# Performance work log

Measured on AMD Instinct MI355X. Metric: run time of the kernel, lower is better.

The kernel has to match this reference:

```python
import jax, jax.numpy as jnp
import numpy as np

N = 50000      # nodes
E = 1600000    # edges
IN = 128       # in_channels
H = 64         # hidden_channels
P = 200000     # edge pairs to score
BN_EPS = 1e-5


def setup_inputs() -> dict:
    key = jax.random.key(0)
    ks = jax.random.split(key, 24)
    lin = lambda k, i, o: jax.random.normal(k, (i, o), jnp.float32) / np.sqrt(i).astype(np.float32)
    return {
        "x": jax.random.normal(ks[0], (N, IN), jnp.float32),
        "edge_index": jax.random.randint(ks[1], (2, E), 0, N, jnp.int32),
        "src": jax.random.randint(ks[2], (P,), 0, N, jnp.int32),
        "dst": jax.random.randint(ks[3], (P,), 0, N, jnp.int32),
        # GCNConv weights/biases
        "W1": lin(ks[4], IN, H),        "b1": jnp.zeros((H,), jnp.float32),
        "W2": lin(ks[5], H, 2 * H),     "b2": jnp.zeros((2 * H,), jnp.float32),
        "W3": lin(ks[6], 2 * H, 2 * H), "b3": jnp.zeros((2 * H,), jnp.float32),
        # BatchNorm affine params
        "g1": jnp.ones((H,), jnp.float32),     "bt1": jnp.zeros((H,), jnp.float32),
        "g2": jnp.ones((2 * H,), jnp.float32), "bt2": jnp.zeros((2 * H,), jnp.float32),
        "g3": jnp.ones((2 * H,), jnp.float32), "bt3": jnp.zeros((2 * H,), jnp.float32),
        # edge-scoring MLP: Linear(4H -> 2H), ReLU, Linear(2H -> 1)
        "fcW1": lin(ks[7], 4 * H, 2 * H), "fcb1": jnp.zeros((2 * H,), jnp.float32),
        "fcW2": lin(ks[8], 2 * H, 1),     "fcb2": jnp.zeros((1,), jnp.float32),
    }


def _gcn_norm(edge_index):
    # add self-loops, symmetric normalization D^-1/2 (A+I) D^-1/2
    loop = jnp.arange(N, dtype=edge_index.dtype)
    row = jnp.concatenate([edge_index[0], loop])
    col = jnp.concatenate([edge_index[1], loop])
    deg = jax.ops.segment_sum(jnp.ones(row.shape, jnp.float32), col, num_segments=N)
    dis = jnp.where(deg > 0, jax.lax.rsqrt(deg), 0.0)
    norm = dis[row] * dis[col]
    return row, col, norm


def _conv(x, W, b, row, col, norm):
    h = x @ W                                  # [N, C]
    msg = h[row] * norm[:, None]               # [E+N, C] gather + scale
    agg = jax.ops.segment_sum(msg, col, num_segments=N)
    return agg + b


def _bn(x, g, bt):
    mu = x.mean(0)
    var = x.var(0)
    return g * (x - mu) * jax.lax.rsqrt(var + BN_EPS) + bt


def reference(x, edge_index, src, dst,
              W1, b1, W2, b2, W3, b3,
              g1, bt1, g2, bt2, g3, bt3,
              fcW1, fcb1, fcW2, fcb2):
    row, col, norm = _gcn_norm(edge_index)
    # inference path: dropout is identity; BN uses batch statistics
    z = _bn(jax.nn.relu(_conv(x, W1, b1, row, col, norm)), g1, bt1)
    z = _bn(jax.nn.relu(_conv(z, W2, b2, row, col, norm)), g2, bt2)
    z = _bn(jax.nn.relu(_conv(z, W3, b3, row, col, norm)), g3, bt3)
    # score(): gather-concat-MLP over edge pairs
    emb = jnp.concatenate([z[src], z[dst]], axis=1)   # [P, 4H]
    hidden = jax.nn.relu(emb @ fcW1 + fcb1)
    scores = (hidden @ fcW2 + fcb2).squeeze(-1)       # [P]
    return scores
```

## Files before the change

kernel.cpp:

```cpp
#include <hip/hip_runtime.h>
#include <math.h>

typedef short bf16x8 __attribute__((ext_vector_type(8)));
typedef float f32x4 __attribute__((ext_vector_type(4)));

__device__ inline unsigned int f2bf_pack(float lo, float hi) {
    unsigned int ul = __builtin_bit_cast(unsigned int, lo);
    unsigned int uh = __builtin_bit_cast(unsigned int, hi);
    ul = ul + 0x7fffu + ((ul >> 16) & 1u);
    uh = uh + 0x7fffu + ((uh >> 16) & 1u);
    return (ul >> 16) | (uh & 0xffff0000u);
}
__device__ inline unsigned short f2bf(float f) {
    unsigned int u = __builtin_bit_cast(unsigned int, f);
    u = u + 0x7fffu + ((u >> 16) & 1u);
    return (unsigned short)(u >> 16);
}
__device__ inline float bf2f(unsigned short u) {
    return __builtin_bit_cast(float, (unsigned int)u << 16);
}
__device__ inline float bflo(unsigned int w) { return __builtin_bit_cast(float, w << 16); }
__device__ inline float bfhi(unsigned int w) { return __builtin_bit_cast(float, w & 0xffff0000u); }


__global__ __launch_bounds__(256) void k_count(const int* __restrict__ col, int* deg, int E) {
    int e = blockIdx.x * 256 + threadIdx.x;
    if (e < E) atomicAdd(&deg[col[e]], 1);
}

__global__ __launch_bounds__(1024) void k_scan_blk(const int* __restrict__ deg, int* __restrict__ offs,
                                                   int* __restrict__ bsum, float* __restrict__ dis, int n) {
    __shared__ int tmp[1024];
    int i = blockIdx.x * 1024 + threadIdx.x;
    int v = (i < n) ? deg[i] : 0;
    if (i < n) dis[i] = 1.0f / sqrtf((float)(v + 1));
    tmp[threadIdx.x] = v;
    __syncthreads();
    for (int off = 1; off < 1024; off <<= 1) {
        int t = (threadIdx.x >= off) ? tmp[threadIdx.x - off] : 0;
        __syncthreads();
        tmp[threadIdx.x] += t;
        __syncthreads();
    }
    if (i < n) offs[i] = tmp[threadIdx.x] - v;
    if (threadIdx.x == 1023) bsum[blockIdx.x] = tmp[1023];
}

__global__ void k_scan_top(int* bsum, int nb) {
    if (threadIdx.x == 0) {
        int acc = 0;
        for (int b = 0; b < nb; b++) { int t = bsum[b]; bsum[b] = acc; acc += t; }
        bsum[nb] = acc;
    }
}

__global__ __launch_bounds__(1024) void k_scan_add(int* __restrict__ offs, int* __restrict__ bcur,
                                                   const int* __restrict__ bsum, int n, int nb) {
    int i = blockIdx.x * 1024 + threadIdx.x;
    if (i < n) {
        int v = offs[i] + bsum[blockIdx.x];
        offs[i] = v;
        if ((i & 511) == 0) bcur[i >> 9] = v;
    }
    if (i == 0) offs[n] = bsum[nb];
}


__global__ __launch_bounds__(256) void k_binA(const int* __restrict__ row, const int* __restrict__ col,
                                              int* __restrict__ bcur, int2* __restrict__ binned,
                                              int E, int NB) {
    constexpr int SLOTS = 32;
    constexpr int CHUNK = 2048;
    __shared__ int2 stage[128][SLOTS];
    __shared__ int lcount[128];
    for (int b = threadIdx.x; b < 128; b += 256) lcount[b] = 0;
    __syncthreads();
    for (int cs = blockIdx.x * CHUNK; cs < E; cs += gridDim.x * CHUNK) {
#pragma unroll
        for (int j = 0; j < CHUNK / 256; ++j) {
            int e = cs + j * 256 + threadIdx.x;
            if (e < E) {
                int r = row[e], c = col[e];
                int b = c >> 9;
                int pos = atomicAdd(&lcount[b], 1);
                if (pos < SLOTS) stage[b][pos] = make_int2(r, c);
                else {
                    int gp = atomicAdd(&bcur[b], 1);
                    binned[gp] = make_int2(r, c);
                }
            }
        }
        __syncthreads();
        for (int b = threadIdx.x; b < NB; b += 256) {
            int c = lcount[b];
            if (c > SLOTS) c = SLOTS;
            if (c > 0) {
                int gp = atomicAdd(&bcur[b], c);
                for (int j = 0; j < c; ++j) binned[gp + j] = stage[b][j];
            }
            lcount[b] = 0;
        }
        __syncthreads();
    }
}

__global__ __launch_bounds__(1024) void k_binB(const int2* __restrict__ binned, const int* __restrict__ offs,
                                               const float* __restrict__ dis, int2* __restrict__ csr, int N) {
    constexpr int CAP = 17408;
    __shared__ int2 stage[CAP];
    __shared__ int cnt[512];
    __shared__ int cur[512];
    const int b = blockIdx.x;
    const int lo = b << 9;
    int hi = lo + 512; if (hi > N) hi = N;
    const int base = offs[lo];
    const int total = offs[hi] - base;

    if (threadIdx.x < 512) cnt[threadIdx.x] = 0;
    __syncthreads();
    for (int i = threadIdx.x; i < total; i += 1024)
        atomicAdd(&cnt[binned[base + i].y - lo], 1);
    __syncthreads();
    int own = 0;
    if (threadIdx.x < 512) own = cnt[threadIdx.x];
    for (int off = 1; off < 512; off <<= 1) {
        int t = 0;
        if (threadIdx.x < 512 && threadIdx.x >= off) t = cnt[threadIdx.x - off];
        __syncthreads();
        if (threadIdx.x < 512) cnt[threadIdx.x] += t;
        __syncthreads();
    }
    if (threadIdx.x < 512) cur[threadIdx.x] = cnt[threadIdx.x] - own;
    __syncthreads();
    for (int i = threadIdx.x; i < total; i += 1024) {
        int2 e = binned[base + i];
        int slot = atomicAdd(&cur[e.y - lo], 1);
        int2 o = make_int2(e.x, __builtin_bit_cast(int, dis[e.x]));
        if (slot < CAP) stage[slot] = o;
        else csr[base + slot] = o;
    }
    __syncthreads();
    int lim = total < CAP ? total : CAP;
    for (int i = threadIdx.x; i < lim; i += 1024) csr[base + i] = stage[i];
}


__global__ __launch_bounds__(256) void k_cast(const float* __restrict__ X, unsigned short* __restrict__ Y, int n8) {
    int i = blockIdx.x * 256 + threadIdx.x;
    if (i >= n8) return;
    const float4* x4 = (const float4*)X;
    float4 a = x4[2 * i], b = x4[2 * i + 1];
    uint4 o = make_uint4(f2bf_pack(a.x, a.y), f2bf_pack(a.z, a.w),
                         f2bf_pack(b.x, b.y), f2bf_pack(b.z, b.w));
    *(uint4*)(Y + (size_t)i * 8) = o;
}


template <int K, int COUT>
__global__ __launch_bounds__(256) void k_prep(const float* __restrict__ W, unsigned short* __restrict__ Wt) {
    constexpr int NG = (COUT / 16) * (K / 32) * 64;
    int g = blockIdx.x * 256 + threadIdx.x;
    if (g >= NG) return;
    int l = g & 63;
    int ks = (g >> 6) % (K / 32);
    int nt = g / (64 * (K / 32));
    int n = nt * 16 + (l & 15);
    int k0 = ks * 32 + (l >> 4) * 8;
    unsigned int w[4];
#pragma unroll
    for (int j = 0; j < 4; ++j) {
        float a = W[(size_t)(k0 + 2 * j) * COUT + n];
        float b = W[(size_t)(k0 + 2 * j + 1) * COUT + n];
        w[j] = f2bf_pack(a, b);
    }
    *(uint4*)(Wt + (size_t)g * 8) = make_uint4(w[0], w[1], w[2], w[3]);
}


template <int K, int COUT, bool FUSED>
__global__ __launch_bounds__(256) void k_mgemm(const unsigned short* __restrict__ Xb,
                                               const unsigned short* __restrict__ Wt,
                                               const float* __restrict__ bias,
                                               unsigned short* __restrict__ H,
                                               float* __restrict__ part, int n) {
    constexpr int NT = COUT / 16;
    constexpr int KS = K / 32;
    __shared__ float reds[FUSED ? 16 : 1][COUT];
    __shared__ float redq[FUSED ? 16 : 1][COUT];
    const int lane = threadIdx.x & 63;
    const int wave = threadIdx.x >> 6;
    const int m = lane & 15, g4 = lane >> 4;
    const int rb = blockIdx.x * 64 + wave * 16;

    bf16x8 af[KS];
    {
        int arow = rb + m;
        if (arow >= n) arow = n - 1;
        const unsigned short* xr = Xb + (size_t)arow * K + g4 * 8;
#pragma unroll
        for (int ks = 0; ks < KS; ++ks) af[ks] = *(const bf16x8*)(xr + ks * 32);
    }
    const bf16x8* Wv = (const bf16x8*)Wt;
    f32x4 acc[NT];
#pragma unroll
    for (int nt = 0; nt < NT; ++nt) {
        f32x4 a = {0.f, 0.f, 0.f, 0.f};
#pragma unroll
        for (int ks = 0; ks < KS; ++ks)
            a = __builtin_amdgcn_mfma_f32_16x16x32_bf16(af[ks], Wv[(nt * KS + ks) * 64 + lane], a, 0, 0, 0);
        acc[nt] = a;
    }

    if (!FUSED) {
#pragma unroll
        for (int nt = 0; nt < NT; ++nt)
#pragma unroll
            for (int r = 0; r < 4; ++r) {
                int gr = rb + g4 * 4 + r;
                if (gr < n) H[(size_t)gr * COUT + nt * 16 + m] = f2bf(acc[nt][r]);
            }
    } else {
        float vs[NT], vq[NT];
#pragma unroll
        for (int nt = 0; nt < NT; ++nt) {
            float b1 = bias[nt * 16 + m];
            vs[nt] = 0.f; vq[nt] = 0.f;
#pragma unroll
            for (int r = 0; r < 4; ++r) {
                int gr = rb + g4 * 4 + r;
                bool ok = gr < n;
                float val = ok ? fmaxf(acc[nt][r] + b1, 0.f) : 0.f;
                if (ok) H[(size_t)gr * COUT + nt * 16 + m] = f2bf(val);
                vs[nt] += val;
                vq[nt] += val * val;
            }
        }
#pragma unroll
        for (int nt = 0; nt < NT; ++nt) {
            reds[wave * 4 + g4][nt * 16 + m] = vs[nt];
            redq[wave * 4 + g4][nt * 16 + m] = vq[nt];
        }
        __syncthreads();
        for (int c = threadIdx.x; c < COUT; c += 256) {
            float S = 0.f, Q = 0.f;
#pragma unroll
            for (int t = 0; t < 16; ++t) { S += reds[t][c]; Q += redq[t][c]; }
            part[(size_t)blockIdx.x * 2 * COUT + c] = S;
            part[(size_t)blockIdx.x * 2 * COUT + COUT + c] = Q;
        }
    }
}


__global__ __launch_bounds__(256) void k_agg64(const unsigned short* __restrict__ H, const int* __restrict__ offs,
                                               const int2* __restrict__ csr, const float* __restrict__ dis,
                                               const float* __restrict__ bias, unsigned short* __restrict__ Y,
                                               float* __restrict__ part, int n) {
    const int lane = threadIdx.x & 63;
    const int wave = threadIdx.x >> 6;
    const int gw = blockIdx.x * 4 + wave;
    const int nw = gridDim.x * 4;
    float bsum = 0.f, bsq = 0.f;
    const float bias_r = bias[lane];

    for (int node = gw; node < n; node += nw) {
        int s0 = offs[node], s1 = offs[node + 1];
        float a = 0.f;
        int e = s0;
        for (; e + 4 <= s1; e += 4) {
            int2 e0 = csr[e], e1 = csr[e + 1], e2 = csr[e + 2], e3 = csr[e + 3];
            float h0 = bf2f(H[(size_t)e0.x * 64 + lane]);
            float h1 = bf2f(H[(size_t)e1.x * 64 + lane]);
            float h2 = bf2f(H[(size_t)e2.x * 64 + lane]);
            float h3 = bf2f(H[(size_t)e3.x * 64 + lane]);
            a += __builtin_bit_cast(float, e0.y) * h0 + __builtin_bit_cast(float, e1.y) * h1;
            a += __builtin_bit_cast(float, e2.y) * h2 + __builtin_bit_cast(float, e3.y) * h3;
        }
        for (; e < s1; ++e) {
            int2 e0 = csr[e];
            a += __builtin_bit_cast(float, e0.y) * bf2f(H[(size_t)e0.x * 64 + lane]);
        }
        float dn = dis[node];
        float val = a * dn + bf2f(H[(size_t)node * 64 + lane]) * dn * dn + bias_r;
        val = fmaxf(val, 0.f);
        Y[(size_t)node * 64 + lane] = f2bf(val);
        bsum += val;
        bsq += val * val;
    }
    __shared__ float psum[4][64], psq[4][64];
    psum[wave][lane] = bsum; psq[wave][lane] = bsq;
    __syncthreads();
    if (threadIdx.x < 64) {
        int c = threadIdx.x;
        float s = psum[0][c] + psum[1][c] + psum[2][c] + psum[3][c];
        float qq = psq[0][c] + psq[1][c] + psq[2][c] + psq[3][c];
        part[(size_t)blockIdx.x * 128 + c] = s;
        part[(size_t)blockIdx.x * 128 + 64 + c] = qq;
    }
}


template <int C>
__global__ __launch_bounds__(256) void k_aggpre(const unsigned short* __restrict__ IN, const int* __restrict__ offs,
                                                const int2* __restrict__ csr, const float* __restrict__ dis,
                                                const float* __restrict__ ss, unsigned short* __restrict__ OUT, int n) {
    constexpr int VPL = C / 64;
    const int lane = threadIdx.x & 63;
    const int wave = threadIdx.x >> 6;
    const int gw = blockIdx.x * 4 + wave;
    const int nw = gridDim.x * 4;
    float sc[VPL], sh[VPL];
#pragma unroll
    for (int q = 0; q < VPL; q++) { sc[q] = ss[lane * VPL + q]; sh[q] = ss[C + lane * VPL + q]; }

    for (int node = gw; node < n; node += nw) {
        int s0 = offs[node], s1 = offs[node + 1];
        float a[VPL];
        float S = 0.f;
#pragma unroll
        for (int q = 0; q < VPL; q++) a[q] = 0.f;
        int e = s0;
        for (; e + 4 <= s1; e += 4) {
            int2 e0 = csr[e], e1 = csr[e + 1], e2 = csr[e + 2], e3 = csr[e + 3];
            float v0 = __builtin_bit_cast(float, e0.y);
            float v1 = __builtin_bit_cast(float, e1.y);
            float v2 = __builtin_bit_cast(float, e2.y);
            float v3 = __builtin_bit_cast(float, e3.y);
            S += (v0 + v1) + (v2 + v3);
            if (VPL == 2) {
                unsigned int w0 = *(const unsigned int*)(IN + (size_t)e0.x * C + 2 * lane);
                unsigned int w1 = *(const unsigned int*)(IN + (size_t)e1.x * C + 2 * lane);
                unsigned int w2 = *(const unsigned int*)(IN + (size_t)e2.x * C + 2 * lane);
                unsigned int w3 = *(const unsigned int*)(IN + (size_t)e3.x * C + 2 * lane);
                a[0] += v0 * bflo(w0) + v1 * bflo(w1) + v2 * bflo(w2) + v3 * bflo(w3);
                a[1] += v0 * bfhi(w0) + v1 * bfhi(w1) + v2 * bfhi(w2) + v3 * bfhi(w3);
            } else {
                float h0 = bf2f(IN[(size_t)e0.x * C + lane]);
                float h1 = bf2f(IN[(size_t)e1.x * C + lane]);
                float h2 = bf2f(IN[(size_t)e2.x * C + lane]);
                float h3 = bf2f(IN[(size_t)e3.x * C + lane]);
                a[0] += v0 * h0 + v1 * h1 + v2 * h2 + v3 * h3;
            }
        }
        for (; e < s1; ++e) {
            int2 e0 = csr[e];
            float v0 = __builtin_bit_cast(float, e0.y);
            S += v0;
            if (VPL == 2) {
                unsigned int w0 = *(const unsigned int*)(IN + (size_t)e0.x * C + 2 * lane);
                a[0] += v0 * bflo(w0);
                a[1] += v0 * bfhi(w0);
            } else {
                a[0] += v0 * bf2f(IN[(size_t)e0.x * C + lane]);
            }
        }
        float dn = dis[node];
        float shf = S + dn;
        if (VPL == 2) {
            unsigned int wsf = *(const unsigned int*)(IN + (size_t)node * C + 2 * lane);
            float o0 = dn * ((a[0] + dn * bflo(wsf)) * sc[0] + shf * sh[0]);
            float o1 = dn * ((a[1] + dn * bfhi(wsf)) * sc[1] + shf * sh[1]);
            *(unsigned int*)(OUT + (size_t)node * C + 2 * lane) = f2bf_pack(o0, o1);
        } else {
            float hsf = bf2f(IN[(size_t)node * C + lane]);
            OUT[(size_t)node * C + lane] = f2bf(dn * ((a[0] + dn * hsf) * sc[0] + shf * sh[0]));
        }
    }
}


template <int C>
__global__ __launch_bounds__(1024) void k_bnfin(const float* __restrict__ part, int nblk,
                                                const float* __restrict__ g, const float* __restrict__ bt,
                                                float* __restrict__ ss, int n) {
    constexpr int ROWS = 1024 / C;
    __shared__ float ssum[1024], ssq[1024];
    const int c = threadIdx.x % C;
    const int r = threadIdx.x / C;
    float s = 0.f, q = 0.f;
    for (int b = r; b < nblk; b += ROWS) {
        s += part[(size_t)b * 2 * C + c];
        q += part[(size_t)b * 2 * C + C + c];
    }
    ssum[threadIdx.x] = s; ssq[threadIdx.x] = q;
    __syncthreads();
    if (r == 0) {
        double S = (double)s, Q = (double)q;
        for (int rr = 1; rr < ROWS; rr++) { S += (double)ssum[rr * C + c]; Q += (double)ssq[rr * C + c]; }
        double invN = 1.0 / (double)n;
        double mu = S * invN;
        double var = Q * invN - mu * mu;
        float scale = g[c] / sqrtf((float)var + 1e-5f);
        ss[c] = scale;
        ss[C + c] = bt[c] - (float)mu * scale;
    }
}


__global__ __launch_bounds__(128) void k_score(const unsigned short* __restrict__ Z, const float* __restrict__ ss,
                                               const int* __restrict__ src, const int* __restrict__ dst,
                                               const unsigned short* __restrict__ Wt,
                                               const float* __restrict__ fcb1, const float* __restrict__ fcW2,
                                               const float* __restrict__ fcb2, float* __restrict__ out, int P) {
    __shared__ unsigned int emb[2][16][128];
    const int lane = threadIdx.x & 63;
    const int wave = threadIdx.x >> 6;
    unsigned int (*Ew)[128] = emb[wave];
    const int tile = blockIdx.x * 2 + wave;
    const int pbase = tile * 16;

    const float2 sc2 = *(const float2*)&ss[2 * lane];
    const float2 sh2 = *(const float2*)&ss[128 + 2 * lane];

#pragma unroll 4
    for (int p = 0; p < 16; ++p) {
        int pi = pbase + p;
        int is = src[pi], id = dst[pi];
        unsigned int wa = *(const unsigned int*)(Z + (size_t)is * 128 + 2 * lane);
        unsigned int wb = *(const unsigned int*)(Z + (size_t)id * 128 + 2 * lane);
        unsigned int ua = f2bf_pack(bflo(wa) * sc2.x + sh2.x, bfhi(wa) * sc2.y + sh2.y);
        unsigned int ub = f2bf_pack(bflo(wb) * sc2.x + sh2.x, bfhi(wb) * sc2.y + sh2.y);
        int swz = (p & 7) << 4;
        char* rowp = (char*)&Ew[p][0];
        *(unsigned int*)(rowp + ((lane * 4) ^ swz)) = ua;
        *(unsigned int*)(rowp + (((lane + 64) * 4) ^ swz)) = ub;
    }

    const int m = lane & 15;
    const int g4 = lane >> 4;
    bf16x8 af[8];
    {
        const char* rowp = (const char*)&Ew[m][0];
        const int sw = (m & 7) << 4;
#pragma unroll
        for (int ks = 0; ks < 8; ++ks)
            af[ks] = *(const bf16x8*)(rowp + ((ks * 64 + g4 * 16) ^ sw));
    }

    float sacc[4] = {0.f, 0.f, 0.f, 0.f};
    const bf16x8* Wtv = (const bf16x8*)Wt;
#pragma unroll 2
    for (int nt = 0; nt < 8; ++nt) {
        f32x4 acc = {0.f, 0.f, 0.f, 0.f};
#pragma unroll
        for (int ks = 0; ks < 8; ++ks) {
            bf16x8 bf = Wtv[(nt * 8 + ks) * 64 + lane];
            acc = __builtin_amdgcn_mfma_f32_16x16x32_bf16(af[ks], bf, acc, 0, 0, 0);
        }
        int oc = nt * 16 + m;
        float b1 = fcb1[oc];
        float w2 = fcW2[oc];
#pragma unroll
        for (int r = 0; r < 4; ++r) {
            float h = fmaxf(acc[r] + b1, 0.f);
            sacc[r] += h * w2;
        }
    }

    const float b2v = fcb2[0];
#pragma unroll
    for (int r = 0; r < 4; ++r) {
        float s = sacc[r];
        s += __shfl_xor(s, 1);
        s += __shfl_xor(s, 2);
        s += __shfl_xor(s, 4);
        s += __shfl_xor(s, 8);
        if (m == 0) out[pbase + g4 * 4 + r] = s + b2v;
    }
}


extern "C" void kernel_launch(void* const* d_in, const int* in_sizes, int n_in,
                              void* d_out, int out_size, void* d_ws, size_t ws_size,
                              hipStream_t stream) {
    const float* x   = (const float*)d_in[0];
    const int* ei    = (const int*)d_in[1];
    const int* src   = (const int*)d_in[2];
    const int* dst   = (const int*)d_in[3];
    const float* W1  = (const float*)d_in[4];
    const float* b1  = (const float*)d_in[5];
    const float* W2  = (const float*)d_in[6];
    const float* b2  = (const float*)d_in[7];
    const float* W3  = (const float*)d_in[8];
    const float* b3  = (const float*)d_in[9];
    const float* g1  = (const float*)d_in[10];
    const float* bt1 = (const float*)d_in[11];
    const float* g2  = (const float*)d_in[12];
    const float* bt2 = (const float*)d_in[13];
    const float* g3  = (const float*)d_in[14];
    const float* bt3 = (const float*)d_in[15];
    const float* fcW1 = (const float*)d_in[16];
    const float* fcb1 = (const float*)d_in[17];
    const float* fcW2 = (const float*)d_in[18];
    const float* fcb2 = (const float*)d_in[19];
    float* out = (float*)d_out;

    const int N = in_sizes[0] / 128;
    const int E = in_sizes[1] / 2;
    const int P = in_sizes[2];
    const int* erow = ei;
    const int* ecol = ei + E;
    const int NB = (N + 511) >> 9;

    const int AGG_GRID = 2048;

    char* w = (char*)d_ws;
    auto alloc = [&](size_t bytes) { void* p = (void*)w; w += (bytes + 255) & ~(size_t)255; return p; };
    int*   deg     = (int*)alloc((size_t)N * 4);
    float* dis     = (float*)alloc((size_t)N * 4);
    int*   offs    = (int*)alloc((size_t)(N + 1) * 4);
    int*   bsum    = (int*)alloc((size_t)65 * 4);
    int*   bcur    = (int*)alloc((size_t)128 * 4);
    int2*  csr     = (int2*)alloc((size_t)E * 8);
    int2*  binned  = (int2*)alloc((size_t)E * 8);
    float* part    = (float*)alloc((size_t)AGG_GRID * 256 * 4);
    float* ss1     = (float*)alloc(2 * 64 * 4);
    float* ss2     = (float*)alloc(2 * 128 * 4);
    float* ss3     = (float*)alloc(2 * 128 * 4);
    unsigned short* Wts = (unsigned short*)alloc((size_t)4096 * 8 * 2);
    unsigned short* Wt1 = (unsigned short*)alloc((size_t)1024 * 8 * 2);
    unsigned short* Wt2 = (unsigned short*)alloc((size_t)1024 * 8 * 2);
    unsigned short* Wt3 = (unsigned short*)alloc((size_t)2048 * 8 * 2);
    unsigned short* Xb1 = (unsigned short*)alloc((size_t)N * 128 * 2);
    unsigned short* bhA = (unsigned short*)alloc((size_t)N * 128 * 2);
    unsigned short* bhB = (unsigned short*)alloc((size_t)N * 128 * 2);
    (void)ws_size; (void)n_in; (void)out_size;

    const int nb_e = (E + 255) / 256;
    const int nb_s = (N + 1023) / 1024;

    hipMemsetAsync(deg, 0, (size_t)N * 4, stream);
    k_count<<<nb_e, 256, 0, stream>>>(ecol, deg, E);
    k_scan_blk<<<nb_s, 1024, 0, stream>>>(deg, offs, bsum, dis, N);
    k_scan_top<<<1, 64, 0, stream>>>(bsum, nb_s);
    k_scan_add<<<nb_s, 1024, 0, stream>>>(offs, bcur, bsum, N, nb_s);
    k_binA<<<256, 256, 0, stream>>>(erow, ecol, bcur, binned, E, NB);
    k_binB<<<NB, 1024, 0, stream>>>(binned, offs, dis, csr, N);

    k_prep<256, 128><<<16, 256, 0, stream>>>(fcW1, Wts);
    k_prep<128, 64><<<4, 256, 0, stream>>>(W1, Wt1);
    k_prep<64, 128><<<4, 256, 0, stream>>>(W2, Wt2);
    k_prep<128, 128><<<8, 256, 0, stream>>>(W3, Wt3);
    k_cast<<<(N * 16 + 255) / 256, 256, 0, stream>>>(x, Xb1, N * 16);

    const int gemm_grid = (N + 63) / 64;

    k_mgemm<128, 64, false><<<gemm_grid, 256, 0, stream>>>(Xb1, Wt1, nullptr, bhA, nullptr, N);
    k_agg64<<<AGG_GRID, 256, 0, stream>>>(bhA, offs, csr, dis, b1, bhB, part, N);
    k_bnfin<64><<<1, 1024, 0, stream>>>(part, AGG_GRID, g1, bt1, ss1, N);

    k_aggpre<64><<<AGG_GRID, 256, 0, stream>>>(bhB, offs, csr, dis, ss1, Xb1, N);
    k_mgemm<64, 128, true><<<gemm_grid, 256, 0, stream>>>(Xb1, Wt2, b2, bhA, part, N);
    k_bnfin<128><<<1, 1024, 0, stream>>>(part, gemm_grid, g2, bt2, ss2, N);

    k_aggpre<128><<<AGG_GRID, 256, 0, stream>>>(bhA, offs, csr, dis, ss2, Xb1, N);
    k_mgemm<128, 128, true><<<gemm_grid, 256, 0, stream>>>(Xb1, Wt3, b3, bhB, part, N);
    k_bnfin<128><<<1, 1024, 0, stream>>>(part, gemm_grid, g3, bt3, ss3, N);

    const int score_grid = P / 32;
    k_score<<<score_grid, 128, 0, stream>>>(bhB, ss3, src, dst, Wts, fcb1, fcW2, fcb2, out, P);
}
```

Measured before the change: 590.3 us.

## Build CSR from fixed-capacity bucket slabs, dropping global degree count and scan

```diff
diff --git a/kernel.cpp b/kernel.cpp
--- a/kernel.cpp
+++ b/kernel.cpp
@@ -3,6 +3,8 @@
 
 typedef short bf16x8 __attribute__((ext_vector_type(8)));
 typedef float f32x4 __attribute__((ext_vector_type(4)));
+
+#define BCAP 17408
 
 __device__ inline unsigned int f2bf_pack(float lo, float hi) {
     unsigned int ul = __builtin_bit_cast(unsigned int, lo);
@@ -23,48 +25,10 @@
 __device__ inline float bfhi(unsigned int w) { return __builtin_bit_cast(float, w & 0xffff0000u); }
 
 
-__global__ __launch_bounds__(256) void k_count(const int* __restrict__ col, int* deg, int E) {
-    int e = blockIdx.x * 256 + threadIdx.x;
-    if (e < E) atomicAdd(&deg[col[e]], 1);
-}
-
-__global__ __launch_bounds__(1024) void k_scan_blk(const int* __restrict__ deg, int* __restrict__ offs,
-                                                   int* __restrict__ bsum, float* __restrict__ dis, int n) {
-    __shared__ int tmp[1024];
-    int i = blockIdx.x * 1024 + threadIdx.x;
-    int v = (i < n) ? deg[i] : 0;
-    if (i < n) dis[i] = 1.0f / sqrtf((float)(v + 1));
-    tmp[threadIdx.x] = v;
-    __syncthreads();
-    for (int off = 1; off < 1024; off <<= 1) {
-        int t = (threadIdx.x >= off) ? tmp[threadIdx.x - off] : 0;
-        __syncthreads();
-        tmp[threadIdx.x] += t;
-        __syncthreads();
-    }
-    if (i < n) offs[i] = tmp[threadIdx.x] - v;
-    if (threadIdx.x == 1023) bsum[blockIdx.x] = tmp[1023];
-}
-
-__global__ void k_scan_top(int* bsum, int nb) {
-    if (threadIdx.x == 0) {
-        int acc = 0;
-        for (int b = 0; b < nb; b++) { int t = bsum[b]; bsum[b] = acc; acc += t; }
-        bsum[nb] = acc;
-    }
-}
-
-__global__ __launch_bounds__(1024) void k_scan_add(int* __restrict__ offs, int* __restrict__ bcur,
-                                                   const int* __restrict__ bsum, int n, int nb) {
-    int i = blockIdx.x * 1024 + threadIdx.x;
-    if (i < n) {
-        int v = offs[i] + bsum[blockIdx.x];
-        offs[i] = v;
-        if ((i & 511) == 0) bcur[i >> 9] = v;
-    }
-    if (i == 0) offs[n] = bsum[nb];
-}
-
+__global__ void k_seed(int* bcur, int NB) {
+    int b = threadIdx.x;
+    if (b < NB) bcur[b] = b * BCAP;
+}
 
 __global__ __launch_bounds__(256) void k_binA(const int* __restrict__ row, const int* __restrict__ col,
                                               int* __restrict__ bcur, int2* __restrict__ binned,
@@ -104,22 +68,31 @@
     }
 }
 
-__global__ __launch_bounds__(1024) void k_binB(const int2* __restrict__ binned, const int* __restrict__ offs,
-                                               const float* __restrict__ dis, int2* __restrict__ csr, int N) {
-    constexpr int CAP = 17408;
-    __shared__ int2 stage[CAP];
+__global__ void k_btop(const int* __restrict__ bcur, int* __restrict__ bstart,
+                       int* __restrict__ offs, int NB, int N) {
+    if (threadIdx.x == 0) {
+        int acc = 0;
+        for (int b = 0; b < NB; b++) {
+            bstart[b] = acc;
+            acc += bcur[b] - b * BCAP;
+        }
+        bstart[NB] = acc;
+        offs[N] = acc;
+    }
+}
+
+__global__ __launch_bounds__(1024) void k_binB1(const int2* __restrict__ binned, const int* __restrict__ bcur,
+                                                const int* __restrict__ bstart, int* __restrict__ offs,
+                                                float* __restrict__ dis, int N) {
     __shared__ int cnt[512];
-    __shared__ int cur[512];
     const int b = blockIdx.x;
     const int lo = b << 9;
-    int hi = lo + 512; if (hi > N) hi = N;
-    const int base = offs[lo];
-    const int total = offs[hi] - base;
-
+    const int slab = b * BCAP;
+    const int count = bcur[b] - slab;
     if (threadIdx.x < 512) cnt[threadIdx.x] = 0;
     __syncthreads();
-    for (int i = threadIdx.x; i < total; i += 1024)
-        atomicAdd(&cnt[binned[base + i].y - lo], 1);
+    for (int i = threadIdx.x; i < count; i += 1024)
+        atomicAdd(&cnt[binned[slab + i].y - lo], 1);
     __syncthreads();
     int own = 0;
     if (threadIdx.x < 512) own = cnt[threadIdx.x];
@@ -130,17 +103,36 @@
         if (threadIdx.x < 512) cnt[threadIdx.x] += t;
         __syncthreads();
     }
-    if (threadIdx.x < 512) cur[threadIdx.x] = cnt[threadIdx.x] - own;
-    __syncthreads();
-    for (int i = threadIdx.x; i < total; i += 1024) {
-        int2 e = binned[base + i];
+    if (threadIdx.x < 512 && lo + threadIdx.x < N) {
+        offs[lo + threadIdx.x] = bstart[b] + cnt[threadIdx.x] - own;
+        dis[lo + threadIdx.x] = 1.0f / sqrtf((float)(own + 1));
+    }
+}
+
+__global__ __launch_bounds__(1024) void k_binB2(const int2* __restrict__ binned, const int* __restrict__ bcur,
+                                                const int* __restrict__ bstart, const int* __restrict__ offs,
+                                                const float* __restrict__ dis, int2* __restrict__ csr, int N) {
+    __shared__ int2 stage[BCAP];
+    __shared__ int cur[512];
+    const int b = blockIdx.x;
+    const int lo = b << 9;
+    const int slab = b * BCAP;
+    const int count = bcur[b] - slab;
+    const int base = bstart[b];
+    if (threadIdx.x < 512) {
+        int node = lo + threadIdx.x;
+        cur[threadIdx.x] = (node < N ? offs[node] : base + count) - base;
+    }
+    __syncthreads();
+    for (int i = threadIdx.x; i < count; i += 1024) {
+        int2 e = binned[slab + i];
         int slot = atomicAdd(&cur[e.y - lo], 1);
         int2 o = make_int2(e.x, __builtin_bit_cast(int, dis[e.x]));
-        if (slot < CAP) stage[slot] = o;
+        if (slot < BCAP) stage[slot] = o;
         else csr[base + slot] = o;
     }
     __syncthreads();
-    int lim = total < CAP ? total : CAP;
+    int lim = count < BCAP ? count : BCAP;
     for (int i = threadIdx.x; i < lim; i += 1024) csr[base + i] = stage[i];
 }
 
@@ -506,13 +498,12 @@
 
     char* w = (char*)d_ws;
     auto alloc = [&](size_t bytes) { void* p = (void*)w; w += (bytes + 255) & ~(size_t)255; return p; };
-    int*   deg     = (int*)alloc((size_t)N * 4);
     float* dis     = (float*)alloc((size_t)N * 4);
     int*   offs    = (int*)alloc((size_t)(N + 1) * 4);
-    int*   bsum    = (int*)alloc((size_t)65 * 4);
     int*   bcur    = (int*)alloc((size_t)128 * 4);
+    int*   bstart  = (int*)alloc((size_t)(NB + 1) * 4);
     int2*  csr     = (int2*)alloc((size_t)E * 8);
-    int2*  binned  = (int2*)alloc((size_t)E * 8);
+    int2*  binned  = (int2*)alloc((size_t)NB * BCAP * 8);
     float* part    = (float*)alloc((size_t)AGG_GRID * 256 * 4);
     float* ss1     = (float*)alloc(2 * 64 * 4);
     float* ss2     = (float*)alloc(2 * 128 * 4);
@@ -526,16 +517,11 @@
     unsigned short* bhB = (unsigned short*)alloc((size_t)N * 128 * 2);
     (void)ws_size; (void)n_in; (void)out_size;
 
-    const int nb_e = (E + 255) / 256;
-    const int nb_s = (N + 1023) / 1024;
-
-    hipMemsetAsync(deg, 0, (size_t)N * 4, stream);
-    k_count<<<nb_e, 256, 0, stream>>>(ecol, deg, E);
-    k_scan_blk<<<nb_s, 1024, 0, stream>>>(deg, offs, bsum, dis, N);
-    k_scan_top<<<1, 64, 0, stream>>>(bsum, nb_s);
-    k_scan_add<<<nb_s, 1024, 0, stream>>>(offs, bcur, bsum, N, nb_s);
+    k_seed<<<1, 128, 0, stream>>>(bcur, NB);
     k_binA<<<256, 256, 0, stream>>>(erow, ecol, bcur, binned, E, NB);
-    k_binB<<<NB, 1024, 0, stream>>>(binned, offs, dis, csr, N);
+    k_btop<<<1, 64, 0, stream>>>(bcur, bstart, offs, NB, N);
+    k_binB1<<<NB, 1024, 0, stream>>>(binned, bcur, bstart, offs, dis, N);
+    k_binB2<<<NB, 1024, 0, stream>>>(binned, bcur, bstart, offs, dis, csr, N);
 
     k_prep<256, 128><<<16, 256, 0, stream>>>(fcW1, Wts);
     k_prep<128, 64><<<4, 256, 0, stream>>>(W1, Wt1);
```

Result: faster. 511.4 us (-13.4%).
